# Performance work log

Hardware: AMD Instinct MI355X
Metric: run time of the kernel (lower is better)

Reference implementation:

```python
import jax, jax.numpy as jnp
import numpy as np

NUM_NODES = 8192
NUM_EDGES = 262144
IN_C = 512
OUT_C = 512


def setup_inputs() -> dict:
    key = jax.random.key(0)
    k1, k2, k3, k4 = jax.random.split(key, 4)
    x = jax.random.normal(k1, (NUM_NODES, IN_C), dtype=jnp.float32)
    edge_index = jax.random.randint(k2, (2, NUM_EDGES), 0, NUM_NODES, dtype=jnp.int64)
    # nn.Linear params (W: [out, in], b: [out]) with kaiming-ish scale
    W = jax.random.normal(k3, (OUT_C, IN_C), dtype=jnp.float32) * (1.0 / np.sqrt(IN_C))
    b = jax.random.normal(k4, (OUT_C,), dtype=jnp.float32) * 0.01
    return {"x": x, "edge_index": edge_index, "W": W, "b": b}


def reference(x, edge_index, W, b):
    n = x.shape[0]
    # append self loops
    loop = jnp.arange(n, dtype=edge_index.dtype)
    rows = jnp.concatenate([edge_index[0], loop])
    cols = jnp.concatenate([edge_index[1], loop])
    # dense adjacency via scatter-set (duplicates collapse to 1.0, matching torch indexing assign)
    adj = jnp.zeros((n, n), dtype=jnp.float32).at[rows, cols].set(1.0)
    deg = adj.sum(axis=1)
    deg_inv_sqrt = jnp.where(deg > 0, jax.lax.rsqrt(jnp.maximum(deg, 1e-30)), 0.0)
    norm = deg_inv_sqrt[:, None] * adj * deg_inv_sqrt[None, :]
    h = x @ W.T + b            # [N, out_c]
    return norm @ h            # [N, out_c]
```

## Files before the change

kernel.cpp:

```cpp
#include <hip/hip_runtime.h>
#include <stdint.h>

#define N_NODES 8192
#define N_EDGES 262144
#define IN_C    512
#define OUT_C   512
#define MAX_DEG 512
#define X_ELEMS (N_NODES * IN_C)
#define W_ELEMS (OUT_C * IN_C)
#define BM_WORDS (N_NODES * (N_NODES / 32))

typedef __attribute__((ext_vector_type(8))) short short8;
typedef __attribute__((ext_vector_type(4))) float f32x4;

__device__ inline uint16_t f2bf(float f) {
    uint32_t u = __float_as_uint(f);
    uint32_t r = (u + 0x7FFFu + ((u >> 16) & 1u)) >> 16;
    return (uint16_t)r;
}

__global__ __launch_bounds__(256) void convert_k(const float* __restrict__ x,
                                                 const float* __restrict__ W,
                                                 uint16_t* __restrict__ xb,
                                                 uint16_t* __restrict__ wb,
                                                 int* __restrict__ cnt,
                                                 uint4* __restrict__ bm) {
    int tid = blockIdx.x * 256 + threadIdx.x;
    if (tid < N_NODES) cnt[tid] = 0;
    if (tid < BM_WORDS / 4) bm[tid] = make_uint4(0u, 0u, 0u, 0u);
    int i = tid * 8;
    const float* src; uint16_t* dst;
    if (i < X_ELEMS) { src = x + i; dst = xb + i; }
    else             { src = W + (i - X_ELEMS); dst = wb + (i - X_ELEMS); }
    float4 v0 = *(const float4*)(src);
    float4 v1 = *(const float4*)(src + 4);
    ushort4 o0, o1;
    o0.x = f2bf(v0.x); o0.y = f2bf(v0.y); o0.z = f2bf(v0.z); o0.w = f2bf(v0.w);
    o1.x = f2bf(v1.x); o1.y = f2bf(v1.y); o1.z = f2bf(v1.z); o1.w = f2bf(v1.w);
    *(ushort4*)(dst)     = o0;
    *(ushort4*)(dst + 4) = o1;
}

__global__ __launch_bounds__(256) void gemm_scatter_k(const uint16_t* __restrict__ xb,
                                                      const uint16_t* __restrict__ wb,
                                                      const float* __restrict__ bias,
                                                      uint16_t* __restrict__ h,
                                                      const int* __restrict__ ei,
                                                      int* __restrict__ cnt,
                                                      uint16_t* __restrict__ nbr,
                                                      uint32_t* __restrict__ bm) {
    const int bid = blockIdx.x;
    if (bid < 512) {
        const int wave = threadIdx.x >> 6;
        const int lane = threadIdx.x & 63;
        const int quad = lane >> 4;
        const int l16  = lane & 15;
        const int mrow = (bid & 7) * 8 + (bid >> 6);
        const int ncol = (bid >> 3) & 7;
        const int m_base = mrow * 128 + (wave & 1) * 64;
        const int n_base = ncol * 64 + (wave >> 1) * 32;

        f32x4 acc[4][2];
        #pragma unroll
        for (int a = 0; a < 4; a++)
            #pragma unroll
            for (int s = 0; s < 2; s++) acc[a][s] = (f32x4){0.f, 0.f, 0.f, 0.f};

        #pragma unroll 2
        for (int k0 = 0; k0 < IN_C; k0 += 32) {
            short8 af[4], bf[2];
            #pragma unroll
            for (int a = 0; a < 4; a++)
                af[a] = *(const short8*)(xb + (m_base + a * 16 + l16) * IN_C + quad * 8 + k0);
            #pragma unroll
            for (int s = 0; s < 2; s++)
                bf[s] = *(const short8*)(wb + (n_base + s * 16 + l16) * IN_C + quad * 8 + k0);
            #pragma unroll
            for (int a = 0; a < 4; a++)
                #pragma unroll
                for (int s = 0; s < 2; s++)
                    acc[a][s] = __builtin_amdgcn_mfma_f32_16x16x32_bf16(bf[s], af[a], acc[a][s], 0, 0, 0);
        }
        #pragma unroll
        for (int s = 0; s < 2; s++) {
            int col_n0 = n_base + s * 16 + quad * 4;
            float4 bv = *(const float4*)(bias + col_n0);
            #pragma unroll
            for (int a = 0; a < 4; a++) {
                int row_m = m_base + a * 16 + l16;
                ushort4 o;
                o.x = f2bf(acc[a][s][0] + bv.x);
                o.y = f2bf(acc[a][s][1] + bv.y);
                o.z = f2bf(acc[a][s][2] + bv.z);
                o.w = f2bf(acc[a][s][3] + bv.w);
                *(ushort4*)(h + row_m * OUT_C + col_n0) = o;
            }
        }
    } else {
        int t = (bid - 512) * 256 + threadIdx.x;
        int r, c;
        if (t < N_EDGES) {
            r = ei[t];
            c = ei[N_EDGES + t];
        } else if (t < N_EDGES + N_NODES) {
            r = t - N_EDGES; c = r;
        } else return;
        uint32_t w   = (uint32_t)r * (uint32_t)(N_NODES / 32) + ((uint32_t)c >> 5);
        uint32_t bit = 1u << (c & 31);
        uint32_t old = atomicOr(&bm[w], bit);
        if (!(old & bit)) {
            int pos = atomicAdd(&cnt[r], 1);
            if (pos < MAX_DEG) nbr[r * MAX_DEG + pos] = (uint16_t)c;
        }
    }
}

__global__ __launch_bounds__(64) void aggregate_k(const int* __restrict__ cnt,
                                                  const uint16_t* __restrict__ nbr,
                                                  const uint32_t* __restrict__ h2,
                                                  float* __restrict__ out) {
    const int i    = blockIdx.x >> 2;
    const int q    = blockIdx.x & 3;
    const int lane = threadIdx.x;
    int m = cnt[i]; if (m > MAX_DEG) m = MAX_DEG;

    __shared__ uint16_t jl[MAX_DEG];
    __shared__ float    dl[MAX_DEG];
    for (int t = lane; t < m; t += 64) {
        uint16_t j = nbr[i * MAX_DEG + t];
        jl[t] = j;
        dl[t] = rsqrtf((float)cnt[j]);
    }
    __syncthreads();

    const uint32_t* hp = h2 + q * 64 + lane;
    float s0 = 0.f, s1 = 0.f;
    #pragma unroll 8
    for (int l = 0; l < m; l++) {
        uint32_t u = hp[(int)jl[l] * 256];
        float dj = dl[l];
        s0 += dj * __uint_as_float(u << 16);
        s1 += dj * __uint_as_float(u & 0xFFFF0000u);
    }
    float di = rsqrtf((float)m);
    int c = q * 128 + lane * 2;
    float2 o = {di * s0, di * s1};
    *(float2*)(out + i * OUT_C + c) = o;
}

extern "C" void kernel_launch(void* const* d_in, const int* in_sizes, int n_in,
                              void* d_out, int out_size, void* d_ws, size_t ws_size,
                              hipStream_t stream) {
    const float* x  = (const float*)d_in[0];
    const int*   ei = (const int*)  d_in[1];
    const float* W  = (const float*)d_in[2];
    const float* b  = (const float*)d_in[3];
    float* out = (float*)d_out;
    char* ws = (char*)d_ws;

    const size_t CNT_OFF = 0;
    const size_t BM_OFF  = 32768;
    const size_t NBR_OFF = BM_OFF + 8388608;
    const size_t XB_OFF  = NBR_OFF + 8388608;
    const size_t WB_OFF  = XB_OFF + 8388608;
    const size_t H_OFF   = WB_OFF + 524288;
    int*      cnt = (int*)     (ws + CNT_OFF);
    uint32_t* bm  = (uint32_t*)(ws + BM_OFF);
    uint16_t* nbr = (uint16_t*)(ws + NBR_OFF);
    uint16_t* xb  = (uint16_t*)(ws + XB_OFF);
    uint16_t* wb  = (uint16_t*)(ws + WB_OFF);
    uint16_t* h   = (uint16_t*)(ws + H_OFF);

    convert_k<<<(X_ELEMS + W_ELEMS) / (256 * 8), 256, 0, stream>>>(x, W, xb, wb, cnt, (uint4*)bm);

    gemm_scatter_k<<<512 + (N_EDGES + N_NODES + 255) / 256, 256, 0, stream>>>(
        xb, wb, b, h, ei, cnt, nbr, bm);

    aggregate_k<<<N_NODES * 4, 64, 0, stream>>>(cnt, nbr, (const uint32_t*)h, out);
}
```

Before: 132.7 us.

## Process four nodes per wave in aggregation and shrink neighbor list capacity

The aggregation kernel moves from one 64-thread block per (node, column-quarter) to 256-thread blocks in which each wave handles four nodes in turn, using a per-wave shared-memory neighbor list and no block barrier. This cuts the block count fourfold and amortizes per-block scheduling and setup cost. MAX_DEG drops from 512 to 128, which shrinks the neighbor buffer and workspace. Nodes with more than 128 unique neighbors would be silently truncated, and correctness relies on wave-lockstep visibility of the shared-memory writes.

```diff
diff --git a/kernel.cpp b/kernel.cpp
--- a/kernel.cpp
+++ b/kernel.cpp
@@ -5,7 +5,7 @@
 #define N_EDGES 262144
 #define IN_C    512
 #define OUT_C   512
-#define MAX_DEG 512
+#define MAX_DEG 128
 #define X_ELEMS (N_NODES * IN_C)
 #define W_ELEMS (OUT_C * IN_C)
 #define BM_WORDS (N_NODES * (N_NODES / 32))
@@ -115,37 +115,45 @@
     }
 }
 
-__global__ __launch_bounds__(64) void aggregate_k(const int* __restrict__ cnt,
-                                                  const uint16_t* __restrict__ nbr,
-                                                  const uint32_t* __restrict__ h2,
-                                                  float* __restrict__ out) {
-    const int i    = blockIdx.x >> 2;
-    const int q    = blockIdx.x & 3;
-    const int lane = threadIdx.x;
-    int m = cnt[i]; if (m > MAX_DEG) m = MAX_DEG;
+__global__ __launch_bounds__(256) void aggregate_k(const int* __restrict__ cnt,
+                                                   const uint16_t* __restrict__ nbr,
+                                                   const uint32_t* __restrict__ h2,
+                                                   float* __restrict__ out) {
+    const int bid  = blockIdx.x;
+    const int w    = threadIdx.x >> 6;
+    const int lane = threadIdx.x & 63;
+    const int q    = bid & 3;
+    const int k    = bid >> 2;
 
-    __shared__ uint16_t jl[MAX_DEG];
-    __shared__ float    dl[MAX_DEG];
-    for (int t = lane; t < m; t += 64) {
-        uint16_t j = nbr[i * MAX_DEG + t];
-        jl[t] = j;
-        dl[t] = rsqrtf((float)cnt[j]);
-    }
-    __syncthreads();
+    __shared__ uint16_t jl[4][MAX_DEG];
+    __shared__ float    dl[4][MAX_DEG];
 
     const uint32_t* hp = h2 + q * 64 + lane;
-    float s0 = 0.f, s1 = 0.f;
-    #pragma unroll 8
-    for (int l = 0; l < m; l++) {
-        uint32_t u = hp[(int)jl[l] * 256];
-        float dj = dl[l];
-        s0 += dj * __uint_as_float(u << 16);
-        s1 += dj * __uint_as_float(u & 0xFFFF0000u);
+
+    #pragma unroll
+    for (int t = 0; t < 4; t++) {
+        const int i = k * 16 + w * 4 + t;
+        int m = cnt[i]; if (m > MAX_DEG) m = MAX_DEG;
+
+        for (int e = lane; e < m; e += 64) {
+            uint16_t j = nbr[i * MAX_DEG + e];
+            jl[w][e] = j;
+            dl[w][e] = rsqrtf((float)cnt[j]);
+        }
+
+        float s0 = 0.f, s1 = 0.f;
+        #pragma unroll 8
+        for (int l = 0; l < m; l++) {
+            uint32_t u = hp[(int)jl[w][l] * 256];
+            float dj = dl[w][l];
+            s0 += dj * __uint_as_float(u << 16);
+            s1 += dj * __uint_as_float(u & 0xFFFF0000u);
+        }
+        float di = rsqrtf((float)m);
+        int c = q * 128 + lane * 2;
+        float2 o = {di * s0, di * s1};
+        *(float2*)(out + i * OUT_C + c) = o;
     }
-    float di = rsqrtf((float)m);
-    int c = q * 128 + lane * 2;
-    float2 o = {di * s0, di * s1};
-    *(float2*)(out + i * OUT_C + c) = o;
 }
 
 extern "C" void kernel_launch(void* const* d_in, const int* in_sizes, int n_in,
@@ -161,7 +169,7 @@
     const size_t CNT_OFF = 0;
     const size_t BM_OFF  = 32768;
     const size_t NBR_OFF = BM_OFF + 8388608;
-    const size_t XB_OFF  = NBR_OFF + 8388608;
+    const size_t XB_OFF  = NBR_OFF + 2097152;
     const size_t WB_OFF  = XB_OFF + 8388608;
     const size_t H_OFF   = WB_OFF + 524288;
     int*      cnt = (int*)     (ws + CNT_OFF);
@@ -176,5 +184,5 @@
     gemm_scatter_k<<<512 + (N_EDGES + N_NODES + 255) / 256, 256, 0, stream>>>(
         xb, wb, b, h, ei, cnt, nbr, bm);
 
-    aggregate_k<<<N_NODES * 4, 64, 0, stream>>>(cnt, nbr, (const uint32_t*)h, out);
+    aggregate_k<<<2048, 256, 0, stream>>>(cnt, nbr, (const uint32_t*)h, out);
 }
```

New measurement: 137.6 us. +3.7%, slower.
